# Optimization experiments

Hardware: AMD Instinct MI355X
Metric: run time of the kernel (lower is better)

Reference implementation:

```python
import jax, jax.numpy as jnp
import numpy as np

HEADS = 16

def _layernorm_LC(x, eps=1e-05):
    # Normalizes jointly over the last TWO dims (L, C), matching the custom LayerNorm.
    mean = jnp.mean(x, axis=(-2, -1), keepdims=True)
    var = jnp.mean((x - mean) ** 2, axis=(-2, -1), keepdims=True) + eps
    return (x - mean) / jnp.sqrt(var)  # affine is identity (ones/zeros)


def setup_inputs() -> dict:
    key = jax.random.key(0)
    ks = jax.random.split(key, 11)
    B, L, D = 2, 2048, 1024
    H = 4 * D
    s = 0.02
    return {
        'x': jax.random.normal(ks[0], (B, L, D), jnp.float32),
        'wq': jax.random.normal(ks[1], (D, D), jnp.float32) * s,
        'bq': jax.random.normal(ks[2], (D,), jnp.float32) * s,
        'wk': jax.random.normal(ks[3], (D, D), jnp.float32) * s,
        'bk': jax.random.normal(ks[4], (D,), jnp.float32) * s,
        'wv': jax.random.normal(ks[5], (D, D), jnp.float32) * s,
        'bv': jax.random.normal(ks[6], (D,), jnp.float32) * s,
        'w1': jax.random.normal(ks[7], (D, H), jnp.float32) * s,
        'b1': jax.random.normal(ks[8], (H,), jnp.float32) * s,
        'w2': jax.random.normal(ks[9], (H, D), jnp.float32) * s,
        'b2': jax.random.normal(ks[10], (D,), jnp.float32) * s,
    }


def reference(x, wq, bq, wk, bk, wv, bv, w1, b1, w2, b2):
    B, L, D = x.shape
    dh = D // HEADS
    # QKV projections
    q = (x @ wq + bq).reshape(B, L, HEADS, dh)
    k = (x @ wk + bk).reshape(B, L, HEADS, dh)
    v = (x @ wv + bv).reshape(B, L, HEADS, dh)
    # batched multi-head attention (equivalent to the per-head Python loop)
    scale = 1.0 / jnp.sqrt(jnp.float32(dh))
    scores = jnp.einsum('blhd,bmhd->bhlm', q, k) * scale
    attn = jax.nn.softmax(scores, axis=-1)
    out = jnp.einsum('bhlm,bmhd->blhd', attn, v).reshape(B, L, D)
    # residual + (L,C) layernorm
    h = _layernorm_LC(x + out)
    # feedforward (dropout is identity in eval)
    ff = jax.nn.relu(h @ w1 + b1) @ w2 + b2
    return _layernorm_LC(h + ff)
```

## Files before the change

### kernel.cpp

```cpp
#include <hip/hip_runtime.h>
#include <hip/hip_bf16.h>

typedef __hip_bfloat16 bf16;
typedef __attribute__((ext_vector_type(8))) short short8;
typedef __attribute__((ext_vector_type(4))) short short4v;
typedef __attribute__((ext_vector_type(4))) float f32x4;

#define CB 2
#define CL 2048
#define CD 1024
#define CH 4096
#define NHEADS 16
#define DH 64

__device__ __forceinline__ short f2bs(float f) {
    __hip_bfloat16 h = __float2bfloat16(f);
    return *reinterpret_cast<short*>(&h);
}
__device__ __forceinline__ float bs2f(short s) {
    __hip_bfloat16 h = *reinterpret_cast<__hip_bfloat16*>(&s);
    return __bfloat162float(h);
}

__device__ __forceinline__ void async_copy16(const short* g, short* l) {
    __builtin_amdgcn_global_load_lds((const __attribute__((address_space(1))) unsigned int*)g,
                                     (__attribute__((address_space(3))) unsigned int*)l,
                                     16, 0, 0);
}

__global__ void pack_bias_kernel(const float* __restrict__ bq, const float* __restrict__ bk,
                                 const float* __restrict__ bv, float* __restrict__ o,
                                 float* __restrict__ stats) {
    int i = blockIdx.x * 256 + threadIdx.x;
    if (i < 16) stats[i] = 0.0f;
    if (i < 3072) o[i] = i < 1024 ? bq[i] : (i < 2048 ? bk[i - 1024] : bv[i - 2048]);
}

__global__ void cvt_x_kernel(const float* __restrict__ x, short* __restrict__ o) {
    const int i = (blockIdx.x * 256 + threadIdx.x) * 4;
    const float4 v = *(const float4*)&x[i];
    short4v s; s[0] = f2bs(v.x); s[1] = f2bs(v.y); s[2] = f2bs(v.z); s[3] = f2bs(v.w);
    *(short4v*)&o[i] = s;
}

__global__ void transpose_cvt(const float* __restrict__ in, short* __restrict__ out,
                              int K, int N, int row_off) {
    __shared__ float T[32][33];
    const int tx = threadIdx.x & 31, ty = threadIdx.x >> 5;
    const int k0 = blockIdx.y * 32, n0 = blockIdx.x * 32;
    #pragma unroll
    for (int i = 0; i < 4; ++i)
        T[ty + i * 8][tx] = in[(size_t)(k0 + ty + i * 8) * N + n0 + tx];
    __syncthreads();
    #pragma unroll
    for (int i = 0; i < 4; ++i)
        out[(size_t)(row_off + n0 + ty + i * 8) * K + k0 + tx] = f2bs(T[tx][ty + i * 8]);
}

__global__ void transpose_qkv(const float* __restrict__ wq, const float* __restrict__ wk,
                              const float* __restrict__ wv, short* __restrict__ out) {
    __shared__ float T[32][33];
    const int z = blockIdx.z;
    const float* in = z == 0 ? wq : (z == 1 ? wk : wv);
    const int row_off = z * 1024;
    const int tx = threadIdx.x & 31, ty = threadIdx.x >> 5;
    const int k0 = blockIdx.y * 32, n0 = blockIdx.x * 32;
    #pragma unroll
    for (int i = 0; i < 4; ++i)
        T[ty + i * 8][tx] = in[(size_t)(k0 + ty + i * 8) * CD + n0 + tx];
    __syncthreads();
    #pragma unroll
    for (int i = 0; i < 4; ++i)
        out[(size_t)(row_off + n0 + ty + i * 8) * CD + k0 + tx] = f2bs(T[tx][ty + i * 8]);
}

template <int BN, int BK, int RELU, int EPI>
__launch_bounds__(256)
__global__ void gemm_mfma(const short* __restrict__ A,
                          const short* __restrict__ Bt,
                          const float* __restrict__ bias,
                          short* __restrict__ C,
                          short* __restrict__ C2,
                          int M, int N, int K,
                          float* __restrict__ stats) {
    constexpr int NT = BN / 32;
    constexpr int KH = BK / 32;
    constexpr int ACH = 16 * BK;
    constexpr int BCH = BN * BK / 8;
    __shared__ short As[128 * BK];
    __shared__ short Bs[BN * BK];
    __shared__ float red[8];

    const int tid = threadIdx.x;
    const int wave = tid >> 6, lane = tid & 63, quad = lane >> 4, lm = lane & 15;
    const int wm = (wave & 1) * 64, wn = (wave >> 1) * (NT * 16);

    const int id = blockIdx.y * gridDim.x + blockIdx.x;
    const int xcd = id & 7, within = id >> 3;
    const int by = xcd * 4 + (within & 3);
    const int bx = within >> 2;
    const int row0 = by * 128, col0 = bx * BN;

    f32x4 acc[4][NT];
    #pragma unroll
    for (int i = 0; i < 4; ++i)
        #pragma unroll
        for (int j = 0; j < NT; ++j) { f32x4 z = {0.f, 0.f, 0.f, 0.f}; acc[i][j] = z; }

    for (int k0 = 0; k0 < K; k0 += BK) {
        #pragma unroll
        for (int t = 0; t < ACH / 256; ++t) {
            const int c = t * 256 + tid;
            const int slab = c >> 9, idx = c & 511;
            const int r = idx >> 2, seg = idx & 3;
            async_copy16(A + (size_t)(row0 + r) * K + k0 + slab * 32 + seg * 8, &As[c * 8]);
        }
        #pragma unroll
        for (int t = 0; t < BCH / 256; ++t) {
            const int c = t * 256 + tid;
            const int slab = c / (BN * 4), idx = c % (BN * 4);
            const int r = idx >> 2, seg = idx & 3;
            async_copy16(Bt + (size_t)(col0 + r) * K + k0 + slab * 32 + seg * 8, &Bs[c * 8]);
        }
        __syncthreads();

        #pragma unroll
        for (int kh = 0; kh < KH; ++kh) {
            short8 af[4], bfr[NT];
            #pragma unroll
            for (int mt = 0; mt < 4; ++mt)
                af[mt] = *(const short8*)&As[kh * 4096 + (wm + mt * 16 + lm) * 32 + quad * 8];
            #pragma unroll
            for (int nt = 0; nt < NT; ++nt)
                bfr[nt] = *(const short8*)&Bs[kh * (BN * 32) + (wn + nt * 16 + lm) * 32 + quad * 8];
            #pragma unroll
            for (int mt = 0; mt < 4; ++mt)
                #pragma unroll
                for (int nt = 0; nt < NT; ++nt)
                    acc[mt][nt] = __builtin_amdgcn_mfma_f32_16x16x32_bf16(af[mt], bfr[nt], acc[mt][nt], 0, 0, 0);
        }
        __syncthreads();
    }

    float s1 = 0.f, s2 = 0.f;
    #pragma unroll
    for (int mt = 0; mt < 4; ++mt) {
        #pragma unroll
        for (int nt = 0; nt < NT; ++nt) {
            const int col = col0 + wn + nt * 16 + lm;
            const float bv = bias[col];
            const int rowb = row0 + wm + mt * 16 + quad * 4;
            if (EPI == 1 && col >= 2048) {
                const int b = row0 >> 11;
                const int l0 = rowb & (CL - 1);
                const int lp = (l0 & ~63) | (l0 & 32) | ((l0 & 12) << 1) | ((l0 & 16) >> 2);
                short4v sv;
                #pragma unroll
                for (int r = 0; r < 4; ++r) sv[r] = f2bs(acc[mt][nt][r] + bv);
                *(short4v*)&C2[(size_t)b * CD * CL + (size_t)(col - 2048) * CL + lp] = sv;
            } else {
                #pragma unroll
                for (int r = 0; r < 4; ++r) {
                    float v = acc[mt][nt][r] + bv;
                    if (RELU) v = fmaxf(v, 0.f);
                    const int ld = (EPI == 1) ? 2048 : N;
                    const size_t idx = (size_t)(rowb + r) * ld + col;
                    if (EPI == 2) {
                        v += bs2f(C[idx]);
                        s1 += v; s2 += v * v;
                    }
                    C[idx] = f2bs(v);
                }
            }
        }
    }
    if (EPI == 2) {
        #pragma unroll
        for (int off = 1; off <= 32; off <<= 1) {
            s1 += __shfl_xor(s1, off, 64);
            s2 += __shfl_xor(s2, off, 64);
        }
        if (lane == 0) { red[wave] = s1; red[4 + wave] = s2; }
        __syncthreads();
        if (tid == 0) {
            const int batch = row0 >> 11;
            atomicAdd(&stats[batch * 2 + 0], red[0] + red[1] + red[2] + red[3]);
            atomicAdd(&stats[batch * 2 + 1], red[4] + red[5] + red[6] + red[7]);
        }
    }
}

__launch_bounds__(512)
__global__ void attn_mfma(const short* __restrict__ qk,
                          const short* __restrict__ vT,
                          const float* __restrict__ x,
                          short* __restrict__ sbuf,
                          float* __restrict__ stats) {
    __shared__ short Ks[2][64 * 64];
    __shared__ short Vs[2][64 * 64];
    __shared__ float red[16];

    const int tid = threadIdx.x;
    const int wave = tid >> 6, lane = tid & 63, quad = lane >> 4, lm = lane & 15;
    const int sx = lm & 7;

    const int id = blockIdx.z * (16 * 16) + blockIdx.y * 16 + blockIdx.x;
    const int xcd = id & 7, rest = id >> 3;
    const int qx = rest & 15, gq = rest >> 4;
    const int g = gq * 8 + xcd;
    const int h = g & 15, b = g >> 4;

    const int hoff = h * DH;
    const size_t rowb = (size_t)b * CL;
    const size_t vbase = (size_t)b * CD * CL + (size_t)hoff * CL;
    const int qbase0 = qx * 128 + wave * 16;

    short8 bq[2];
    #pragma unroll
    for (int kf = 0; kf < 2; ++kf)
        bq[kf] = *(const short8*)(qk + (rowb + qbase0 + lm) * 2048 + hoff + kf * 32 + quad * 8);

    f32x4 oacc[4];
    #pragma unroll
    for (int mt = 0; mt < 4; ++mt) { f32x4 z = {0.f, 0.f, 0.f, 0.f}; oacc[mt] = z; }
    float lsum = 0.f;

    auto stage = [&](int buf, int kt) {
        {
            const int key = tid >> 3, sp = tid & 7;
            async_copy16(qk + (rowb + kt * 64 + key) * 2048 + 1024 + hoff + ((sp ^ (key & 7)) * 8),
                         &Ks[buf][tid * 8]);
        }
        {
            const int row = tid >> 3, sp = tid & 7;
            async_copy16(vT + vbase + (size_t)row * CL + kt * 64 + ((sp ^ (row & 7)) * 8),
                         &Vs[buf][tid * 8]);
        }
    };

    stage(0, 0);
    __syncthreads();
    int cur = 0;

    for (int kt = 0; kt < CL / 64; ++kt) {
        if (kt + 1 < CL / 64) stage(cur ^ 1, kt + 1);
        const short* K_ = &Ks[cur][0];
        const short* V_ = &Vs[cur][0];

        float st[4][4];
        #pragma unroll
        for (int ktile = 0; ktile < 4; ++ktile) {
            const int krow = ktile * 16 + lm;
            const int s0 = (quad ^ sx) << 3;
            const short8 a0 = *(const short8*)&K_[krow * 64 + s0];
            const short8 a1 = *(const short8*)&K_[krow * 64 + (s0 ^ 32)];
            f32x4 s = {0.f, 0.f, 0.f, 0.f};
            __builtin_amdgcn_s_setprio(1);
            s = __builtin_amdgcn_mfma_f32_16x16x32_bf16(a0, bq[0], s, 0, 0, 0);
            s = __builtin_amdgcn_mfma_f32_16x16x32_bf16(a1, bq[1], s, 0, 0, 0);
            __builtin_amdgcn_s_setprio(0);
            #pragma unroll
            for (int r = 0; r < 4; ++r) {
                const float p = __expf(s[r] * 0.125f);
                lsum += p;
                st[ktile][r] = p;
            }
        }

        #pragma unroll
        for (int p = 0; p < 2; ++p) {
            short8 pf;
            #pragma unroll
            for (int r = 0; r < 4; ++r) {
                pf[r]     = f2bs(st[2 * p][r]);
                pf[4 + r] = f2bs(st[2 * p + 1][r]);
            }
            #pragma unroll
            for (int mt = 0; mt < 4; ++mt) {
                const int sc = (p * 4 + quad) ^ sx;
                const short8 vf = *(const short8*)&V_[(mt * 16 + lm) * 64 + sc * 8];
                __builtin_amdgcn_s_setprio(1);
                oacc[mt] = __builtin_amdgcn_mfma_f32_16x16x32_bf16(vf, pf, oacc[mt], 0, 0, 0);
                __builtin_amdgcn_s_setprio(0);
            }
        }
        __syncthreads();
        cur ^= 1;
    }

    lsum += __shfl_xor(lsum, 16, 64);
    lsum += __shfl_xor(lsum, 32, 64);

    float s1 = 0.f, s2 = 0.f;
    {
        const float inv = 1.0f / lsum;
        const size_t grow = rowb + qbase0 + lm;
        #pragma unroll
        for (int mt = 0; mt < 4; ++mt) {
            const size_t base = grow * CD + hoff + mt * 16 + quad * 4;
            const float4 xv = *(const float4*)&x[base];
            const float xa[4] = {xv.x, xv.y, xv.z, xv.w};
            short4v sv;
            #pragma unroll
            for (int r = 0; r < 4; ++r) {
                const float s = xa[r] + oacc[mt][r] * inv;
                s1 += s; s2 += s * s;
                sv[r] = f2bs(s);
            }
            *(short4v*)&sbuf[base] = sv;
        }
    }
    #pragma unroll
    for (int off = 1; off <= 32; off <<= 1) {
        s1 += __shfl_xor(s1, off, 64);
        s2 += __shfl_xor(s2, off, 64);
    }
    if (lane == 0) { red[wave] = s1; red[8 + wave] = s2; }
    __syncthreads();
    if (tid == 0) {
        float t1 = 0.f, t2 = 0.f;
        #pragma unroll
        for (int w = 0; w < 8; ++w) { t1 += red[w]; t2 += red[8 + w]; }
        atomicAdd(&stats[b * 2 + 0], t1);
        atomicAdd(&stats[b * 2 + 1], t2);
    }
}

template <typename TO>
__global__ void ln_apply(const short* __restrict__ s, const float* __restrict__ stats,
                         TO* __restrict__ out, int perBatch) {
    const int bId = blockIdx.y;
    const size_t base = (size_t)bId * perBatch;
    const float n = (float)perBatch;
    const float mean = stats[bId * 2 + 0] / n;
    const float var  = stats[bId * 2 + 1] / n - mean * mean + 1e-5f;
    const float inv  = rsqrtf(var);
    const int stride = gridDim.x * 256 * 8;
    for (int i = (blockIdx.x * 256 + threadIdx.x) * 8; i < perBatch; i += stride) {
        const short8 v8 = *(const short8*)&s[base + i];
        float o[8];
        #pragma unroll
        for (int j = 0; j < 8; ++j) o[j] = (bs2f(v8[j]) - mean) * inv;
        if (sizeof(TO) == 4) {
            float4 f0 = {o[0], o[1], o[2], o[3]}, f1 = {o[4], o[5], o[6], o[7]};
            *(float4*)&((float*)out)[base + i] = f0;
            *(float4*)&((float*)out)[base + i + 4] = f1;
        } else {
            short8 r;
            #pragma unroll
            for (int j = 0; j < 8; ++j) r[j] = f2bs(o[j]);
            *(short8*)&((short*)out)[base + i] = r;
        }
    }
}

extern "C" void kernel_launch(void* const* d_in, const int* in_sizes, int n_in,
                              void* d_out, int out_size, void* d_ws, size_t ws_size,
                              hipStream_t stream) {
    const float* x  = (const float*)d_in[0];
    const float* wq = (const float*)d_in[1];
    const float* bq = (const float*)d_in[2];
    const float* wk = (const float*)d_in[3];
    const float* bk = (const float*)d_in[4];
    const float* wv = (const float*)d_in[5];
    const float* bv = (const float*)d_in[6];
    const float* w1 = (const float*)d_in[7];
    const float* b1 = (const float*)d_in[8];
    const float* w2 = (const float*)d_in[9];
    const float* b2 = (const float*)d_in[10];

    const int BL = CB * CL;
    const int perBatch = CL * CD;

    char* ws = (char*)d_ws;
    const size_t MB = 1024 * 1024;
    short* Wqkvt = (short*)(ws);
    float* bqkv  = (float*)(ws + 6 * MB);
    short* w1t   = (short*)(ws);
    short* w2t   = (short*)(ws);
    short* xbf   = (short*)(ws + 8 * MB);
    short* qkb   = (short*)(ws + 16 * MB);
    short* vT    = (short*)(ws + 32 * MB);
    short* ff1   = (short*)(ws + 8 * MB);
    short* hbuf  = (short*)(ws + 40 * MB);
    float* stats = (float*)(ws + 48 * MB);

    dim3 blk(256);

    pack_bias_kernel<<<12, blk, 0, stream>>>(bq, bk, bv, bqkv, stats);
    cvt_x_kernel<<<BL * CD / 1024, blk, 0, stream>>>(x, xbf);
    transpose_qkv<<<dim3(32, 32, 3), blk, 0, stream>>>(wq, wk, wv, Wqkvt);

    gemm_mfma<128, 64, 0, 1><<<dim3(3072 / 128, BL / 128), blk, 0, stream>>>(
        xbf, Wqkvt, bqkv, qkb, vT, BL, 3072, CD, nullptr);

    attn_mfma<<<dim3(CL / 128, NHEADS, CB), dim3(512), 0, stream>>>(qkb, vT, x, hbuf, stats);

    ln_apply<bf16><<<dim3(128, CB), blk, 0, stream>>>(hbuf, stats, (bf16*)hbuf, perBatch);

    transpose_cvt<<<dim3(128, 32), blk, 0, stream>>>(w1, w1t, CD, CH, 0);
    gemm_mfma<128, 64, 1, 0><<<dim3(CH / 128, BL / 128), blk, 0, stream>>>(
        hbuf, w1t, b1, ff1, nullptr, BL, CH, CD, nullptr);

    transpose_cvt<<<dim3(32, 128), blk, 0, stream>>>(w2, w2t, CH, CD, 0);
    gemm_mfma<64, 128, 0, 2><<<dim3(CD / 64, BL / 128), blk, 0, stream>>>(
        ff1, w2t, b2, hbuf, nullptr, BL, CD, CH, stats + 8);

    ln_apply<float><<<dim3(128, CB), blk, 0, stream>>>(hbuf, stats + 8, (float*)d_out, perBatch);
}
```

Before: 345.6 us.

## Load K and V fragments directly from global memory in attention kernel

Removes the double-buffered LDS staging of K and V tiles and the per-iteration block barrier. Each wave now loads its MFMA operand fragments straight from global memory into registers, relying on L2/L1 caching for reuse across the 8 waves of a block. This drops the LDS traffic and synchronisation, but each wave issues eight times as many global loads, loses the prefetch overlap, and uses strided 16-byte accesses.

```diff
diff --git a/kernel.cpp b/kernel.cpp
--- a/kernel.cpp
+++ b/kernel.cpp
@@ -196,13 +196,10 @@
                           const float* __restrict__ x,
                           short* __restrict__ sbuf,
                           float* __restrict__ stats) {
-    __shared__ short Ks[2][64 * 64];
-    __shared__ short Vs[2][64 * 64];
     __shared__ float red[16];
 
     const int tid = threadIdx.x;
     const int wave = tid >> 6, lane = tid & 63, quad = lane >> 4, lm = lane & 15;
-    const int sx = lm & 7;
 
     const int id = blockIdx.z * (16 * 16) + blockIdx.y * 16 + blockIdx.x;
     const int xcd = id & 7, rest = id >> 3;
@@ -225,39 +222,25 @@
     for (int mt = 0; mt < 4; ++mt) { f32x4 z = {0.f, 0.f, 0.f, 0.f}; oacc[mt] = z; }
     float lsum = 0.f;
 
-    auto stage = [&](int buf, int kt) {
-        {
-            const int key = tid >> 3, sp = tid & 7;
-            async_copy16(qk + (rowb + kt * 64 + key) * 2048 + 1024 + hoff + ((sp ^ (key & 7)) * 8),
-                         &Ks[buf][tid * 8]);
-        }
-        {
-            const int row = tid >> 3, sp = tid & 7;
-            async_copy16(vT + vbase + (size_t)row * CL + kt * 64 + ((sp ^ (row & 7)) * 8),
-                         &Vs[buf][tid * 8]);
-        }
-    };
-
-    stage(0, 0);
-    __syncthreads();
-    int cur = 0;
+    const short* kbase = qk + (rowb + lm) * 2048 + 1024 + hoff + quad * 8;
+    const short* vbp   = vT + vbase + (size_t)lm * CL + quad * 8;
 
     for (int kt = 0; kt < CL / 64; ++kt) {
-        if (kt + 1 < CL / 64) stage(cur ^ 1, kt + 1);
-        const short* K_ = &Ks[cur][0];
-        const short* V_ = &Vs[cur][0];
+        const short* kb = kbase + (size_t)kt * 64 * 2048;
+        short8 ka[8];
+        #pragma unroll
+        for (int ktile = 0; ktile < 4; ++ktile) {
+            ka[2 * ktile]     = *(const short8*)(kb + (size_t)ktile * 16 * 2048);
+            ka[2 * ktile + 1] = *(const short8*)(kb + (size_t)ktile * 16 * 2048 + 32);
+        }
 
         float st[4][4];
         #pragma unroll
         for (int ktile = 0; ktile < 4; ++ktile) {
-            const int krow = ktile * 16 + lm;
-            const int s0 = (quad ^ sx) << 3;
-            const short8 a0 = *(const short8*)&K_[krow * 64 + s0];
-            const short8 a1 = *(const short8*)&K_[krow * 64 + (s0 ^ 32)];
             f32x4 s = {0.f, 0.f, 0.f, 0.f};
             __builtin_amdgcn_s_setprio(1);
-            s = __builtin_amdgcn_mfma_f32_16x16x32_bf16(a0, bq[0], s, 0, 0, 0);
-            s = __builtin_amdgcn_mfma_f32_16x16x32_bf16(a1, bq[1], s, 0, 0, 0);
+            s = __builtin_amdgcn_mfma_f32_16x16x32_bf16(ka[2 * ktile], bq[0], s, 0, 0, 0);
+            s = __builtin_amdgcn_mfma_f32_16x16x32_bf16(ka[2 * ktile + 1], bq[1], s, 0, 0, 0);
             __builtin_amdgcn_s_setprio(0);
             #pragma unroll
             for (int r = 0; r < 4; ++r) {
@@ -267,6 +250,14 @@
             }
         }
 
+        const short* vb = vbp + kt * 64;
+        short8 va[8];
+        #pragma unroll
+        for (int p = 0; p < 2; ++p)
+            #pragma unroll
+            for (int mt = 0; mt < 4; ++mt)
+                va[p * 4 + mt] = *(const short8*)(vb + (size_t)(mt * 16) * CL + p * 32);
+
         #pragma unroll
         for (int p = 0; p < 2; ++p) {
             short8 pf;
@@ -275,17 +266,12 @@
                 pf[r]     = f2bs(st[2 * p][r]);
                 pf[4 + r] = f2bs(st[2 * p + 1][r]);
             }
-            #pragma unroll
-            for (int mt = 0; mt < 4; ++mt) {
-                const int sc = (p * 4 + quad) ^ sx;
-                const short8 vf = *(const short8*)&V_[(mt * 16 + lm) * 64 + sc * 8];
-                __builtin_amdgcn_s_setprio(1);
-                oacc[mt] = __builtin_amdgcn_mfma_f32_16x16x32_bf16(vf, pf, oacc[mt], 0, 0, 0);
-                __builtin_amdgcn_s_setprio(0);
-            }
-        }
-        __syncthreads();
-        cur ^= 1;
+            __builtin_amdgcn_s_setprio(1);
+            #pragma unroll
+            for (int mt = 0; mt < 4; ++mt)
+                oacc[mt] = __builtin_amdgcn_mfma_f32_16x16x32_bf16(va[p * 4 + mt], pf, oacc[mt], 0, 0, 0);
+            __builtin_amdgcn_s_setprio(0);
+        }
     }
 
     lsum += __shfl_xor(lsum, 16, 64);
```

Result: slower. 512.0 us (+48.2%).
